# Optimization experiments

Hardware: AMD Instinct MI355X
Metric: run time of the kernel (lower is better)

Reference implementation:

```python
import jax, jax.numpy as jnp
import numpy as np

N, C, S, B = 200000, 128, 6, 2   # nodes, n_ls, n_scales_ls, n_blk
E, E2 = 200000, 100000           # pre/suc edges per scale, left/right edges
EPS = 1e-5

def gn(x, g, b):
    # GroupNorm with 1 group on [N, C]: normalize each row over channels (biased var)
    m = x.mean(axis=-1, keepdims=True)
    v = x.var(axis=-1, keepdims=True)
    return (x - m) * jax.lax.rsqrt(v + EPS) * g + b

def setup_inputs() -> dict:
    key = jax.random.key(0)
    ks = iter(jax.random.split(key, 64))
    nrm = lambda shape, s=0.02: jax.random.normal(next(ks), shape, jnp.float32) * s
    ri = lambda shape: jax.random.randint(next(ks), shape, 0, N, dtype=jnp.int32)
    return dict(
        ctrs=nrm((N, 2), 1.0), feats=nrm((N, 2), 1.0),
        pre_u=ri((S, E)), pre_v=ri((S, E)),
        suc_u=ri((S, E)), suc_v=ri((S, E)),
        left_u=ri((E2,)), left_v=ri((E2,)),
        right_u=ri((E2,)), right_v=ri((E2,)),
        W_in1=nrm((2, C)), b_in1=jnp.zeros((C,), jnp.float32), W_in2=nrm((C, C)),
        g_in=jnp.ones((C,), jnp.float32), bb_in=jnp.zeros((C,), jnp.float32),
        W_seg1=nrm((2, C)), b_seg1=jnp.zeros((C,), jnp.float32), W_seg2=nrm((C, C)),
        g_seg=jnp.ones((C,), jnp.float32), bb_seg=jnp.zeros((C,), jnp.float32),
        W_ctr=nrm((B, C, C)), W_pre=nrm((B, S, C, C)), W_suc=nrm((B, S, C, C)),
        W_left=nrm((B, C, C)), W_right=nrm((B, C, C)),
        g_norm=jnp.ones((B, C), jnp.float32), b_norm=jnp.zeros((B, C), jnp.float32),
        W_ctr2=nrm((B, C, C)),
        g_ctr2=jnp.ones((B, C), jnp.float32), b_ctr2=jnp.zeros((B, C), jnp.float32),
    )

def reference(ctrs, feats, pre_u, pre_v, suc_u, suc_v, left_u, left_v, right_u, right_v,
              W_in1, b_in1, W_in2, g_in, bb_in,
              W_seg1, b_seg1, W_seg2, g_seg, bb_seg,
              W_ctr, W_pre, W_suc, W_left, W_right,
              g_norm, b_norm, W_ctr2, g_ctr2, b_ctr2):
    # input/seg stems: Linear(2,C)+ReLU, then bias-free Linear(C,C)+GroupNorm(1,C)
    feat = gn(jax.nn.relu(ctrs @ W_in1 + b_in1) @ W_in2, g_in, bb_in)
    feat = feat + gn(jax.nn.relu(feats @ W_seg1 + b_seg1) @ W_seg2, g_seg, bb_seg)
    feat = jax.nn.relu(feat)
    res = feat
    for i in range(B):                       # fusion blocks (structural loop)
        temp = feat @ W_ctr[i]               # [N, C]
        for s in range(S):                   # dilation scales (structural loop)
            temp = temp.at[pre_u[s]].add(feat[pre_v[s]] @ W_pre[i, s])
            temp = temp.at[suc_u[s]].add(feat[suc_v[s]] @ W_suc[i, s])
        temp = temp.at[left_u].add(feat[left_v] @ W_left[i])
        temp = temp.at[right_u].add(feat[right_v] @ W_right[i])
        feat = jax.nn.relu(gn(temp, g_norm[i], b_norm[i]))
        feat = gn(feat @ W_ctr2[i], g_ctr2[i], b_ctr2[i])   # ctr2: Linear+GN, no act
        feat = jax.nn.relu(feat + res)
        res = feat
    return feat
```

## Files before the change

### kernel.cpp

```cpp
#include <hip/hip_runtime.h>

#define C 128
#define EPS 1e-5f

typedef __bf16 bf16x8 __attribute__((ext_vector_type(8)));
typedef float f32x4 __attribute__((ext_vector_type(4)));

__device__ __forceinline__ unsigned short f2bf(float f) {
    unsigned int u = __float_as_uint(f);
    unsigned int r = (u + 0x7FFFu + ((u >> 16) & 1u)) >> 16;
    return (unsigned short)r;
}

struct WPtrs { const float* p[34]; };

__global__ __launch_bounds__(128) void convert_weights(WPtrs wp, unsigned short* __restrict__ WT)
{
    int m = blockIdx.y, k = blockIdx.x, c = threadIdx.x;
    float val = wp.p[m][k * C + c];
    WT[((size_t)m * C + c) * C + k] = f2bf(val);
}

__global__ __launch_bounds__(256) void stem_pre(const float* __restrict__ in2,
    const float* __restrict__ W1, const float* __restrict__ b1,
    unsigned short* __restrict__ H, int N)
{
    int idx = blockIdx.x * 256 + threadIdx.x;
    if (idx >= N * C) return;
    int n = idx >> 7, c = idx & 127;
    float h = fmaxf(0.f, fmaf(in2[2 * n], W1[c], fmaf(in2[2 * n + 1], W1[C + c], b1[c])));
    H[idx] = f2bf(h);
}

__global__ __launch_bounds__(256) void gemm_dense(const unsigned short* __restrict__ X,
    const unsigned short* __restrict__ WT, float* __restrict__ Y, int N)
{
    __shared__ unsigned short Xs[128][136];
    __shared__ unsigned short Ws[128][136];
    int tid = threadIdx.x;
    int base = blockIdx.x * 128;

    {
        int r = tid >> 1, h = (tid & 1) * 64;
        int gr = base + r; if (gr >= N) gr = N - 1;
        const uint4* src = (const uint4*)(X + (size_t)gr * C + h);
        uint4* dst = (uint4*)(&Xs[r][h]);
        #pragma unroll
        for (int it = 0; it < 8; ++it) dst[it] = src[it];
    }
    {
        int r = tid >> 1, h = (tid & 1) * 64;
        const uint4* src = (const uint4*)(WT + (size_t)r * C + h);
        uint4* dst = (uint4*)(&Ws[r][h]);
        #pragma unroll
        for (int it = 0; it < 8; ++it) dst[it] = src[it];
    }
    __syncthreads();

    int w = tid >> 6, l = tid & 63;
    int lr = l & 15, lk = (l >> 4) * 8;
    f32x4 acc[2][8];
    #pragma unroll
    for (int m = 0; m < 2; ++m)
        #pragma unroll
        for (int n = 0; n < 8; ++n) acc[m][n] = (f32x4){0.f, 0.f, 0.f, 0.f};

    #pragma unroll
    for (int kk = 0; kk < 4; ++kk) {
        bf16x8 a0 = *(const bf16x8*)&Xs[w * 32 + lr][kk * 32 + lk];
        bf16x8 a1 = *(const bf16x8*)&Xs[w * 32 + 16 + lr][kk * 32 + lk];
        #pragma unroll
        for (int n = 0; n < 8; ++n) {
            bf16x8 b = *(const bf16x8*)&Ws[n * 16 + lr][kk * 32 + lk];
            acc[0][n] = __builtin_amdgcn_mfma_f32_16x16x32_bf16(a0, b, acc[0][n], 0, 0, 0);
            acc[1][n] = __builtin_amdgcn_mfma_f32_16x16x32_bf16(a1, b, acc[1][n], 0, 0, 0);
        }
    }

    #pragma unroll
    for (int m = 0; m < 2; ++m)
        #pragma unroll
        for (int n = 0; n < 8; ++n)
            #pragma unroll
            for (int q = 0; q < 4; ++q) {
                int row = base + w * 32 + m * 16 + (l >> 4) * 4 + q;
                if (row < N) Y[(size_t)row * C + n * 16 + lr] = acc[m][n][q];
            }
}

__global__ __launch_bounds__(256) void edge_gemm(const unsigned short* __restrict__ featB,
    const int* __restrict__ pre_u, const int* __restrict__ pre_v,
    const int* __restrict__ suc_u, const int* __restrict__ suc_v,
    const int* __restrict__ left_u, const int* __restrict__ left_v,
    const int* __restrict__ right_u, const int* __restrict__ right_v,
    const unsigned short* __restrict__ WTb,
    float* __restrict__ T, int E, int E2)
{
    int set = blockIdx.y;
    const int *u, *v; int len; const unsigned short* Wt;
    if (set < 6)       { u = pre_u + (size_t)set * E;       v = pre_v + (size_t)set * E;       len = E; }
    else if (set < 12) { u = suc_u + (size_t)(set - 6) * E; v = suc_v + (size_t)(set - 6) * E; len = E; }
    else if (set == 12){ u = left_u;  v = left_v;  len = E2; }
    else               { u = right_u; v = right_v; len = E2; }
    Wt = WTb + (size_t)(1 + set) * C * C;

    int base = blockIdx.x * 128;
    if (base >= len) return;

    __shared__ unsigned short Xs[128][136];
    __shared__ unsigned short Ws[128][136];
    __shared__ int us[128];

    int tid = threadIdx.x;
    if (tid < 128) us[tid] = (base + tid < len) ? u[base + tid] : -1;
    {
        int r = tid >> 1, h = (tid & 1) * 64;
        int e = base + r;
        int vv = (e < len) ? v[e] : 0;
        const uint4* src = (const uint4*)(featB + (size_t)vv * C + h);
        uint4* dst = (uint4*)(&Xs[r][h]);
        #pragma unroll
        for (int it = 0; it < 8; ++it) dst[it] = src[it];
    }
    {
        int r = tid >> 1, h = (tid & 1) * 64;
        const uint4* src = (const uint4*)(Wt + (size_t)r * C + h);
        uint4* dst = (uint4*)(&Ws[r][h]);
        #pragma unroll
        for (int it = 0; it < 8; ++it) dst[it] = src[it];
    }
    __syncthreads();

    int w = tid >> 6, l = tid & 63;
    int lr = l & 15, lk = (l >> 4) * 8;
    f32x4 acc[2][8];
    #pragma unroll
    for (int m = 0; m < 2; ++m)
        #pragma unroll
        for (int n = 0; n < 8; ++n) acc[m][n] = (f32x4){0.f, 0.f, 0.f, 0.f};

    #pragma unroll
    for (int kk = 0; kk < 4; ++kk) {
        bf16x8 a0 = *(const bf16x8*)&Xs[w * 32 + lr][kk * 32 + lk];
        bf16x8 a1 = *(const bf16x8*)&Xs[w * 32 + 16 + lr][kk * 32 + lk];
        #pragma unroll
        for (int n = 0; n < 8; ++n) {
            bf16x8 b = *(const bf16x8*)&Ws[n * 16 + lr][kk * 32 + lk];
            acc[0][n] = __builtin_amdgcn_mfma_f32_16x16x32_bf16(a0, b, acc[0][n], 0, 0, 0);
            acc[1][n] = __builtin_amdgcn_mfma_f32_16x16x32_bf16(a1, b, acc[1][n], 0, 0, 0);
        }
    }

    #pragma unroll
    for (int m = 0; m < 2; ++m)
        #pragma unroll
        for (int q = 0; q < 4; ++q) {
            int rl = w * 32 + m * 16 + (l >> 4) * 4 + q;
            int dst = us[rl];
            if (dst >= 0) {
                #pragma unroll
                for (int n = 0; n < 8; ++n)
                    atomicAdd(&T[(size_t)dst * C + n * 16 + lr], acc[m][n][q]);
            }
        }
}

__device__ __forceinline__ float grp_sum(float v, int tid, float* red) {
    for (int off = 32; off; off >>= 1) v += __shfl_down(v, off, 64);
    __syncthreads();
    if ((tid & 63) == 0) red[tid >> 6] = v;
    __syncthreads();
    int grp = tid >> 7;
    return red[grp * 2] + red[grp * 2 + 1];
}

__global__ __launch_bounds__(256) void stem_gnA(const float* __restrict__ Y,
    const float* __restrict__ g, const float* __restrict__ b, float* __restrict__ A)
{
    __shared__ float red[4];
    int tid = threadIdx.x;
    int n = blockIdx.x * 2 + (tid >> 7), c = tid & 127;
    size_t idx = (size_t)n * C + c;
    float y = Y[idx];
    float m = grp_sum(y, tid, red) * (1.f / C);
    float d = y - m;
    float var = grp_sum(d * d, tid, red) * (1.f / C);
    A[idx] = d * rsqrtf(var + EPS) * g[c] + b[c];
}

__global__ __launch_bounds__(256) void stem_gnB(const float* __restrict__ Y,
    const float* __restrict__ g, const float* __restrict__ b,
    float* __restrict__ A, unsigned short* __restrict__ featB)
{
    __shared__ float red[4];
    int tid = threadIdx.x;
    int n = blockIdx.x * 2 + (tid >> 7), c = tid & 127;
    size_t idx = (size_t)n * C + c;
    float y = Y[idx];
    float m = grp_sum(y, tid, red) * (1.f / C);
    float d = y - m;
    float var = grp_sum(d * d, tid, red) * (1.f / C);
    float o = d * rsqrtf(var + EPS) * g[c] + b[c];
    float r = fmaxf(0.f, A[idx] + o);
    A[idx] = r;
    featB[idx] = f2bf(r);
}

__global__ __launch_bounds__(256) void tail_gn1(const float* __restrict__ T,
    const float* __restrict__ g, const float* __restrict__ b, unsigned short* __restrict__ Xb)
{
    __shared__ float red[4];
    int tid = threadIdx.x;
    int n = blockIdx.x * 2 + (tid >> 7), c = tid & 127;
    size_t idx = (size_t)n * C + c;
    float y = T[idx];
    float m = grp_sum(y, tid, red) * (1.f / C);
    float d = y - m;
    float var = grp_sum(d * d, tid, red) * (1.f / C);
    Xb[idx] = f2bf(fmaxf(0.f, d * rsqrtf(var + EPS) * g[c] + b[c]));
}

__global__ __launch_bounds__(256) void tail_gn2(float* __restrict__ Y,
    const float* __restrict__ g, const float* __restrict__ b,
    float* __restrict__ A, unsigned short* __restrict__ featB)
{
    __shared__ float red[4];
    int tid = threadIdx.x;
    int n = blockIdx.x * 2 + (tid >> 7), c = tid & 127;
    size_t idx = (size_t)n * C + c;
    float y = Y[idx];
    float m = grp_sum(y, tid, red) * (1.f / C);
    float d = y - m;
    float var = grp_sum(d * d, tid, red) * (1.f / C);
    float o = d * rsqrtf(var + EPS) * g[c] + b[c];
    float r = fmaxf(0.f, A[idx] + o);
    A[idx] = r;
    featB[idx] = f2bf(r);
    Y[idx] = r;
}

extern "C" void kernel_launch(void* const* d_in, const int* in_sizes, int n_in,
                              void* d_out, int out_size, void* d_ws, size_t ws_size,
                              hipStream_t stream)
{
    const float* ctrs   = (const float*)d_in[0];
    const float* feats  = (const float*)d_in[1];
    const int*   pre_u  = (const int*)d_in[2];
    const int*   pre_v  = (const int*)d_in[3];
    const int*   suc_u  = (const int*)d_in[4];
    const int*   suc_v  = (const int*)d_in[5];
    const int*   left_u = (const int*)d_in[6];
    const int*   left_v = (const int*)d_in[7];
    const int*   right_u= (const int*)d_in[8];
    const int*   right_v= (const int*)d_in[9];
    const float* W_in1  = (const float*)d_in[10];
    const float* b_in1  = (const float*)d_in[11];
    const float* W_in2  = (const float*)d_in[12];
    const float* g_in   = (const float*)d_in[13];
    const float* bb_in  = (const float*)d_in[14];
    const float* W_seg1 = (const float*)d_in[15];
    const float* b_seg1 = (const float*)d_in[16];
    const float* W_seg2 = (const float*)d_in[17];
    const float* g_seg  = (const float*)d_in[18];
    const float* bb_seg = (const float*)d_in[19];
    const float* W_ctr  = (const float*)d_in[20];
    const float* W_pre  = (const float*)d_in[21];
    const float* W_suc  = (const float*)d_in[22];
    const float* W_left = (const float*)d_in[23];
    const float* W_right= (const float*)d_in[24];
    const float* g_norm = (const float*)d_in[25];
    const float* b_norm = (const float*)d_in[26];
    const float* W_ctr2 = (const float*)d_in[27];
    const float* g_ctr2 = (const float*)d_in[28];
    const float* b_ctr2 = (const float*)d_in[29];

    const int N  = in_sizes[0] / 2;
    const int S  = 6;
    const int E  = in_sizes[2] / S;
    const int E2 = in_sizes[6];
    const int B  = in_sizes[20] / (C * C);
    const int CC = C * C;

    float* A = (float*)d_ws;
    unsigned short* featB = (unsigned short*)(A + (size_t)N * C);
    unsigned short* WT = featB + (size_t)N * C;
    float* T = (float*)d_out;

    WPtrs wp;
    wp.p[0] = W_in2; wp.p[1] = W_seg2;
    for (int i = 0; i < B; ++i) {
        int base = 2 + i * 16;
        wp.p[base + 0] = W_ctr + (size_t)i * CC;
        for (int s = 0; s < S; ++s) {
            wp.p[base + 1 + s] = W_pre + ((size_t)i * S + s) * CC;
            wp.p[base + 7 + s] = W_suc + ((size_t)i * S + s) * CC;
        }
        wp.p[base + 13] = W_left  + (size_t)i * CC;
        wp.p[base + 14] = W_right + (size_t)i * CC;
        wp.p[base + 15] = W_ctr2  + (size_t)i * CC;
    }

    const int GT = (N + 127) / 128;
    const int GE = (E + 127) / 128;
    dim3 b256(256), b128(128);

    convert_weights<<<dim3(128, 34), b128, 0, stream>>>(wp, WT);

    stem_pre<<<(N * C + 255) / 256, b256, 0, stream>>>(ctrs, W_in1, b_in1, featB, N);
    gemm_dense<<<GT, b256, 0, stream>>>(featB, WT + 0 * (size_t)CC, T, N);
    stem_gnA<<<N / 2, b256, 0, stream>>>(T, g_in, bb_in, A);
    stem_pre<<<(N * C + 255) / 256, b256, 0, stream>>>(feats, W_seg1, b_seg1, featB, N);
    gemm_dense<<<GT, b256, 0, stream>>>(featB, WT + 1 * (size_t)CC, T, N);
    stem_gnB<<<N / 2, b256, 0, stream>>>(T, g_seg, bb_seg, A, featB);

    for (int i = 0; i < B; ++i) {
        const unsigned short* WTb = WT + (size_t)(2 + i * 16) * CC;
        gemm_dense<<<GT, b256, 0, stream>>>(featB, WTb, T, N);
        edge_gemm<<<dim3(GE, 14), b256, 0, stream>>>(featB,
            pre_u, pre_v, suc_u, suc_v, left_u, left_v, right_u, right_v,
            WTb, T, E, E2);
        tail_gn1<<<N / 2, b256, 0, stream>>>(T, g_norm + (size_t)i * C, b_norm + (size_t)i * C, featB);
        gemm_dense<<<GT, b256, 0, stream>>>(featB, WTb + 15 * (size_t)CC, T, N);
        tail_gn2<<<N / 2, b256, 0, stream>>>(T, g_ctr2 + (size_t)i * C, b_ctr2 + (size_t)i * C, A, featB);
    }
}
```

Before: 2.997 ms.

## Sort edges into per-destination CSR and fuse ctr GEMM with edge aggregation

Builds a CSR (histogram, three-stage scan, scatter) of edges grouped by destination node for each of the 14 edge sets, once per call. A new fused kernel handles a tile of 64 destination nodes: it computes the center GEMM, then for each edge set gathers source rows, runs MFMA, and accumulates into a shared-memory tile using LDS atomics before writing T once. This replaces the global float atomics and the separate dense ctr GEMM, at the cost of extra preprocessing kernels, serialized per-set loops with binary searches, and load imbalance across blocks. The CSR is rebuilt on every call rather than cached.

```diff
diff --git a/kernel.cpp b/kernel.cpp
--- a/kernel.cpp
+++ b/kernel.cpp
@@ -19,6 +19,82 @@
     int m = blockIdx.y, k = blockIdx.x, c = threadIdx.x;
     float val = wp.p[m][k * C + c];
     WT[((size_t)m * C + c) * C + k] = f2bf(val);
+}
+
+
+__global__ __launch_bounds__(256) void hist_k(const int* __restrict__ pre_u,
+    const int* __restrict__ suc_u, const int* __restrict__ left_u, const int* __restrict__ right_u,
+    int* __restrict__ deg, int E, int E2, int N)
+{
+    int cs = blockIdx.y;
+    const int* u; int len;
+    if (cs < 6)       { u = pre_u + (size_t)cs * E;       len = E; }
+    else if (cs < 12) { u = suc_u + (size_t)(cs - 6) * E; len = E; }
+    else if (cs == 12){ u = left_u;  len = E2; }
+    else              { u = right_u; len = E2; }
+    int e = blockIdx.x * 256 + threadIdx.x;
+    if (e < len) atomicAdd(&deg[(size_t)cs * N + u[e]], 1);
+}
+
+__global__ __launch_bounds__(256) void scan1(const int* __restrict__ deg, int* __restrict__ off,
+                                             int* __restrict__ bsum, int M)
+{
+    __shared__ int ts[256];
+    int b = blockIdx.x, t = threadIdx.x;
+    int base = b * 4096 + t * 16;
+    int v[16]; int s = 0;
+    #pragma unroll
+    for (int j = 0; j < 16; ++j) { int idx = base + j; int x = (idx < M) ? deg[idx] : 0; v[j] = s; s += x; }
+    ts[t] = s; __syncthreads();
+    for (int o = 1; o < 256; o <<= 1) {
+        int x = (t >= o) ? ts[t - o] : 0;
+        __syncthreads(); ts[t] += x; __syncthreads();
+    }
+    int texcl = (t == 0) ? 0 : ts[t - 1];
+    if (t == 255) bsum[b] = ts[255];
+    #pragma unroll
+    for (int j = 0; j < 16; ++j) { int idx = base + j; if (idx < M) off[idx] = texcl + v[j]; }
+}
+
+__global__ void scan2(int* __restrict__ bsum, int nb)
+{
+    __shared__ int s[1024];
+    int t = threadIdx.x;
+    for (int i = t; i < 1024; i += 256) s[i] = (i < nb) ? bsum[i] : 0;
+    __syncthreads();
+    if (t == 0) { int run = 0; for (int i = 0; i < nb; ++i) { int x = s[i]; s[i] = run; run += x; } }
+    __syncthreads();
+    for (int i = t; i < nb; i += 256) bsum[i] = s[i];
+}
+
+__global__ __launch_bounds__(256) void scan3(int* __restrict__ off, int* __restrict__ cursor,
+                                             const int* __restrict__ bsum, int M)
+{
+    int i = blockIdx.x * 256 + threadIdx.x;
+    if (i >= M) return;
+    int val = off[i] + bsum[i >> 12];
+    int dg = cursor[i];
+    off[i] = val; cursor[i] = val;
+    if (i == M - 1) off[M] = val + dg;
+}
+
+__global__ __launch_bounds__(256) void scatter_k(const int* __restrict__ pre_u, const int* __restrict__ pre_v,
+    const int* __restrict__ suc_u, const int* __restrict__ suc_v,
+    const int* __restrict__ left_u, const int* __restrict__ left_v,
+    const int* __restrict__ right_u, const int* __restrict__ right_v,
+    int* __restrict__ cursor, int* __restrict__ payload, int E, int E2, int N)
+{
+    int cs = blockIdx.y;
+    const int *u, *v; int len;
+    if (cs < 6)       { u = pre_u + (size_t)cs * E;       v = pre_v + (size_t)cs * E;       len = E; }
+    else if (cs < 12) { u = suc_u + (size_t)(cs - 6) * E; v = suc_v + (size_t)(cs - 6) * E; len = E; }
+    else if (cs == 12){ u = left_u;  v = left_v;  len = E2; }
+    else              { u = right_u; v = right_v; len = E2; }
+    int e = blockIdx.x * 256 + threadIdx.x;
+    if (e < len) {
+        int pos = atomicAdd(&cursor[(size_t)cs * N + u[e]], 1);
+        payload[pos] = v[e];
+    }
 }
 
 __global__ __launch_bounds__(256) void stem_pre(const float* __restrict__ in2,
@@ -88,81 +164,117 @@
             }
 }
 
-__global__ __launch_bounds__(256) void edge_gemm(const unsigned short* __restrict__ featB,
-    const int* __restrict__ pre_u, const int* __restrict__ pre_v,
-    const int* __restrict__ suc_u, const int* __restrict__ suc_v,
-    const int* __restrict__ left_u, const int* __restrict__ left_v,
-    const int* __restrict__ right_u, const int* __restrict__ right_v,
-    const unsigned short* __restrict__ WTb,
-    float* __restrict__ T, int E, int E2)
-{
-    int set = blockIdx.y;
-    const int *u, *v; int len; const unsigned short* Wt;
-    if (set < 6)       { u = pre_u + (size_t)set * E;       v = pre_v + (size_t)set * E;       len = E; }
-    else if (set < 12) { u = suc_u + (size_t)(set - 6) * E; v = suc_v + (size_t)(set - 6) * E; len = E; }
-    else if (set == 12){ u = left_u;  v = left_v;  len = E2; }
-    else               { u = right_u; v = right_v; len = E2; }
-    Wt = WTb + (size_t)(1 + set) * C * C;
-
-    int base = blockIdx.x * 128;
-    if (base >= len) return;
-
-    __shared__ unsigned short Xs[128][136];
-    __shared__ unsigned short Ws[128][136];
-    __shared__ int us[128];
-
-    int tid = threadIdx.x;
-    if (tid < 128) us[tid] = (base + tid < len) ? u[base + tid] : -1;
+__device__ __forceinline__ void load_b(const unsigned short* wt, bf16x8 (&bfr)[2][4], int w, int l)
+{
+    int lr = l & 15, lk = (l >> 4) * 8;
+    #pragma unroll
+    for (int nn = 0; nn < 2; ++nn)
+        #pragma unroll
+        for (int kk = 0; kk < 4; ++kk)
+            bfr[nn][kk] = *(const bf16x8*)(wt + ((size_t)((w * 2 + nn) * 16 + lr)) * C + kk * 32 + lk);
+}
+
+__device__ __forceinline__ void mfma_accum(const unsigned short (&Xs)[64][136],
+    float (&acc)[65][132], const int (&ldl)[64], const bf16x8 (&bfr)[2][4], int w, int l)
+{
+    int lr = l & 15, lk = (l >> 4) * 8;
+    #pragma unroll
+    for (int m = 0; m < 4; ++m) {
+        bf16x8 a[4];
+        #pragma unroll
+        for (int kk = 0; kk < 4; ++kk)
+            a[kk] = *(const bf16x8*)&Xs[m * 16 + lr][kk * 32 + lk];
+        f32x4 acc2[2];
+        acc2[0] = (f32x4){0.f, 0.f, 0.f, 0.f};
+        acc2[1] = (f32x4){0.f, 0.f, 0.f, 0.f};
+        #pragma unroll
+        for (int nn = 0; nn < 2; ++nn)
+            #pragma unroll
+            for (int kk = 0; kk < 4; ++kk)
+                acc2[nn] = __builtin_amdgcn_mfma_f32_16x16x32_bf16(a[kk], bfr[nn][kk], acc2[nn], 0, 0, 0);
+        int dls[4];
+        #pragma unroll
+        for (int q = 0; q < 4; ++q) dls[q] = ldl[m * 16 + (l >> 4) * 4 + q];
+        #pragma unroll
+        for (int nn = 0; nn < 2; ++nn) {
+            int ch = (w * 2 + nn) * 16 + lr;
+            #pragma unroll
+            for (int q = 0; q < 4; ++q)
+                atomicAdd(&acc[dls[q]][ch], acc2[nn][q]);
+        }
+    }
+}
+
+__global__ __launch_bounds__(256) void fused_edge(const unsigned short* __restrict__ featB,
+    const int* __restrict__ payload, const int* __restrict__ off,
+    const unsigned short* __restrict__ WTb, float* __restrict__ T, int N)
+{
+    __shared__ float acc[65][132];
+    __shared__ unsigned short Xs[64][136];
+    __shared__ int soff[65];
+    __shared__ int ldl[64];
+
+    int tid = threadIdx.x;
+    int w = tid >> 6, l = tid & 63;
+    int base = blockIdx.x * 64;
+    int r = tid >> 2, part = tid & 3;
+
     {
-        int r = tid >> 1, h = (tid & 1) * 64;
-        int e = base + r;
-        int vv = (e < len) ? v[e] : 0;
-        const uint4* src = (const uint4*)(featB + (size_t)vv * C + h);
-        uint4* dst = (uint4*)(&Xs[r][h]);
-        #pragma unroll
-        for (int it = 0; it < 8; ++it) dst[it] = src[it];
-    }
+        float4* az = (float4*)&acc[0][0];
+        #pragma unroll
+        for (int i = 0; i < 9; ++i) {
+            int idx = tid + i * 256;
+            if (idx < 65 * 33) az[idx] = make_float4(0.f, 0.f, 0.f, 0.f);
+        }
+    }
+
+    bf16x8 bfr[2][4];
+
+    load_b(WTb, bfr, w, l);
+    if (part == 0) ldl[r] = r;
     {
-        int r = tid >> 1, h = (tid & 1) * 64;
-        const uint4* src = (const uint4*)(Wt + (size_t)r * C + h);
-        uint4* dst = (uint4*)(&Ws[r][h]);
-        #pragma unroll
-        for (int it = 0; it < 8; ++it) dst[it] = src[it];
-    }
-    __syncthreads();
-
-    int w = tid >> 6, l = tid & 63;
-    int lr = l & 15, lk = (l >> 4) * 8;
-    f32x4 acc[2][8];
-    #pragma unroll
-    for (int m = 0; m < 2; ++m)
-        #pragma unroll
-        for (int n = 0; n < 8; ++n) acc[m][n] = (f32x4){0.f, 0.f, 0.f, 0.f};
-
-    #pragma unroll
-    for (int kk = 0; kk < 4; ++kk) {
-        bf16x8 a0 = *(const bf16x8*)&Xs[w * 32 + lr][kk * 32 + lk];
-        bf16x8 a1 = *(const bf16x8*)&Xs[w * 32 + 16 + lr][kk * 32 + lk];
-        #pragma unroll
-        for (int n = 0; n < 8; ++n) {
-            bf16x8 b = *(const bf16x8*)&Ws[n * 16 + lr][kk * 32 + lk];
-            acc[0][n] = __builtin_amdgcn_mfma_f32_16x16x32_bf16(a0, b, acc[0][n], 0, 0, 0);
-            acc[1][n] = __builtin_amdgcn_mfma_f32_16x16x32_bf16(a1, b, acc[1][n], 0, 0, 0);
+        const uint4* sp = (const uint4*)(featB + (size_t)(base + r) * C + part * 32);
+        uint4* dp = (uint4*)&Xs[r][part * 32];
+        #pragma unroll
+        for (int j = 0; j < 4; ++j) dp[j] = sp[j];
+    }
+    __syncthreads();
+    mfma_accum(Xs, acc, ldl, bfr, w, l);
+    __syncthreads();
+
+    for (int cs = 0; cs < 14; ++cs) {
+        __syncthreads();
+        if (tid < 65) soff[tid] = off[(size_t)cs * N + base + tid];
+        load_b(WTb + (size_t)(cs + 1) * C * C, bfr, w, l);
+        __syncthreads();
+        int cb = soff[0], end = soff[64];
+        for (int cstart = cb; cstart < end; cstart += 64) {
+            int p = cstart + r;
+            int src = 0, dl = 64;
+            if (p < end) {
+                src = payload[p];
+                int lo = 0, hi = 64;
+                while (hi - lo > 1) { int mid = (lo + hi) >> 1; if (soff[mid] <= p) lo = mid; else hi = mid; }
+                dl = lo;
+            }
+            if (part == 0) ldl[r] = dl;
+            const uint4* sp = (const uint4*)(featB + (size_t)src * C + part * 32);
+            uint4* dp = (uint4*)&Xs[r][part * 32];
+            #pragma unroll
+            for (int j = 0; j < 4; ++j) dp[j] = sp[j];
+            __syncthreads();
+            mfma_accum(Xs, acc, ldl, bfr, w, l);
+            __syncthreads();
         }
     }
 
-    #pragma unroll
-    for (int m = 0; m < 2; ++m)
-        #pragma unroll
-        for (int q = 0; q < 4; ++q) {
-            int rl = w * 32 + m * 16 + (l >> 4) * 4 + q;
-            int dst = us[rl];
-            if (dst >= 0) {
-                #pragma unroll
-                for (int n = 0; n < 8; ++n)
-                    atomicAdd(&T[(size_t)dst * C + n * 16 + lr], acc[m][n][q]);
-            }
-        }
+    __syncthreads();
+    {
+        int d = tid >> 2, co = (tid & 3) * 32;
+        float4* tr = (float4*)(T + (size_t)(base + d) * C + co);
+        #pragma unroll
+        for (int j = 0; j < 8; ++j) tr[j] = *(const float4*)&acc[d][co + j * 4];
+    }
 }
 
 __device__ __forceinline__ float grp_sum(float v, int tid, float* red) {
@@ -280,31 +392,46 @@
     const int E2 = in_sizes[6];
     const int B  = in_sizes[20] / (C * C);
     const int CC = C * C;
+    const int M  = 14 * N;
+    const int ET = 12 * E + 2 * E2;
 
     float* A = (float*)d_ws;
     unsigned short* featB = (unsigned short*)(A + (size_t)N * C);
     unsigned short* WT = featB + (size_t)N * C;
+    int* off     = (int*)(WT + (size_t)34 * CC);
+    int* cursor  = off + (M + 4);
+    int* payload = cursor + M;
+    int* bsum    = payload + ET;
     float* T = (float*)d_out;
 
     WPtrs wp;
     wp.p[0] = W_in2; wp.p[1] = W_seg2;
     for (int i = 0; i < B; ++i) {
-        int base = 2 + i * 16;
-        wp.p[base + 0] = W_ctr + (size_t)i * CC;
+        int wbase = 2 + i * 16;
+        wp.p[wbase + 0] = W_ctr + (size_t)i * CC;
         for (int s = 0; s < S; ++s) {
-            wp.p[base + 1 + s] = W_pre + ((size_t)i * S + s) * CC;
-            wp.p[base + 7 + s] = W_suc + ((size_t)i * S + s) * CC;
+            wp.p[wbase + 1 + s] = W_pre + ((size_t)i * S + s) * CC;
+            wp.p[wbase + 7 + s] = W_suc + ((size_t)i * S + s) * CC;
         }
-        wp.p[base + 13] = W_left  + (size_t)i * CC;
-        wp.p[base + 14] = W_right + (size_t)i * CC;
-        wp.p[base + 15] = W_ctr2  + (size_t)i * CC;
+        wp.p[wbase + 13] = W_left  + (size_t)i * CC;
+        wp.p[wbase + 14] = W_right + (size_t)i * CC;
+        wp.p[wbase + 15] = W_ctr2  + (size_t)i * CC;
     }
 
     const int GT = (N + 127) / 128;
-    const int GE = (E + 127) / 128;
+    const int GEx = (E + 255) / 256;
+    const int NB_SCAN = (M + 4095) / 4096;
     dim3 b256(256), b128(128);
 
     convert_weights<<<dim3(128, 34), b128, 0, stream>>>(wp, WT);
+
+    hipMemsetAsync(cursor, 0, (size_t)M * 4, stream);
+    hist_k<<<dim3(GEx, 14), b256, 0, stream>>>(pre_u, suc_u, left_u, right_u, cursor, E, E2, N);
+    scan1<<<NB_SCAN, b256, 0, stream>>>(cursor, off, bsum, M);
+    scan2<<<1, b256, 0, stream>>>(bsum, NB_SCAN);
+    scan3<<<(M + 255) / 256, b256, 0, stream>>>(off, cursor, bsum, M);
+    scatter_k<<<dim3(GEx, 14), b256, 0, stream>>>(pre_u, pre_v, suc_u, suc_v,
+        left_u, left_v, right_u, right_v, cursor, payload, E, E2, N);
 
     stem_pre<<<(N * C + 255) / 256, b256, 0, stream>>>(ctrs, W_in1, b_in1, featB, N);
     gemm_dense<<<GT, b256, 0, stream>>>(featB, WT + 0 * (size_t)CC, T, N);
@@ -315,10 +442,7 @@
 
     for (int i = 0; i < B; ++i) {
         const unsigned short* WTb = WT + (size_t)(2 + i * 16) * CC;
-        gemm_dense<<<GT, b256, 0, stream>>>(featB, WTb, T, N);
-        edge_gemm<<<dim3(GE, 14), b256, 0, stream>>>(featB,
-            pre_u, pre_v, suc_u, suc_v, left_u, left_v, right_u, right_v,
-            WTb, T, E, E2);
+        fused_edge<<<N / 64, b256, 0, stream>>>(featB, payload, off, WTb, T, N);
         tail_gn1<<<N / 2, b256, 0, stream>>>(T, g_norm + (size_t)i * C, b_norm + (size_t)i * C, featB);
         gemm_dense<<<GT, b256, 0, stream>>>(featB, WTb + 15 * (size_t)CC, T, N);
         tail_gn2<<<N / 2, b256, 0, stream>>>(T, g_ctr2 + (size_t)i * C, b_ctr2 + (size_t)i * C, A, featB);
```

After: 7.080 ms. 136% more time.
